# Kernel tuning notes

Hardware: AMD Instinct MI355X
Metric: run time of the kernel (lower is better)

Reference implementation:

```python
import jax, jax.numpy as jnp
import numpy as np
import math

N, N0, M, K, CIN, COUT, DIM = 50000, 50000, 32, 15, 64, 64, 3
POINT_INFLUENCE = 0.05
KERNEL_RADIUS = 1.5 * POINT_INFLUENCE  # _INFLUENCE_TO_RADIUS * point_influence


def setup_inputs() -> dict:
    key = jax.random.key(0)
    k1, k2, k3, k4, k5, k6 = jax.random.split(key, 6)
    query_points = jax.random.uniform(k1, (N, DIM), dtype=jnp.float32)
    support_points = jax.random.uniform(k2, (N0, DIM), dtype=jnp.float32)
    # index N0 is the shadow-neighbor index (padding for ragged neighborhoods)
    neighbors = jax.random.randint(k3, (N, M), 0, N0 + 1)
    x = jax.random.normal(k4, (N0, CIN), dtype=jnp.float32)
    # kernel point dispositions inside the kernel ball, center point at origin (fixed='center')
    kp = jax.random.normal(k5, (K, DIM), dtype=jnp.float32)
    kp = kp / jnp.linalg.norm(kp, axis=1, keepdims=True) * (KERNEL_RADIUS * 0.66)
    K_points = kp.at[0].set(0.0)
    # xavier_normal_ init for weight [K, CIN, COUT]
    std = math.sqrt(2.0 / (CIN + COUT))
    weight = jax.random.normal(k6, (K, CIN, COUT), dtype=jnp.float32) * std
    return dict(query_points=query_points, support_points=support_points,
                neighbors=neighbors, x=x, K_points=K_points, weight=weight)


def reference(query_points, support_points, neighbors, x, K_points, weight):
    # shadow point far away + zero shadow feature (handles padded neighbor index N0)
    shadow_pt = jnp.full((1, support_points.shape[1]), 1e6, support_points.dtype)
    sp = jnp.concatenate([support_points, shadow_pt], axis=0)          # [N0+1, 3]
    feats = jnp.concatenate([x, jnp.zeros((1, x.shape[1]), x.dtype)], axis=0)  # [N0+1, CIN]

    # gather & center neighborhoods: [N, M, 3]
    nb_pts = sp[neighbors] - query_points[:, None, :]

    # squared distance to each kernel point without materializing [N,M,K,3]:
    # ||n - k||^2 = ||n||^2 - 2 n.k + ||k||^2  -> [N, M, K]
    sq = (jnp.sum(nb_pts * nb_pts, axis=-1)[:, :, None]
          - 2.0 * jnp.einsum('nmd,kd->nmk', nb_pts, K_points)
          + jnp.sum(K_points * K_points, axis=-1))
    sq = jnp.maximum(sq, 0.0)

    # linear KP influence: clamp(1 - dist / point_influence, min=0) -> transpose to [N, K, M]
    all_weights = jnp.maximum(1.0 - jnp.sqrt(sq) / POINT_INFLUENCE, 0.0)
    all_weights = jnp.swapaxes(all_weights, 1, 2)                      # [N, K, M]

    nb_feats = feats[neighbors]                                        # [N, M, CIN]
    weighted = jnp.matmul(all_weights, nb_feats)                       # [N, K, CIN]
    # sum over kernel points of per-kernel-point matmuls ('sum' aggregation)
    out = jnp.einsum('nkc,kco->no', weighted, weight)                  # [N, COUT]
    return out
```

## Files before the change

### kernel.cpp

```cpp
#include <hip/hip_runtime.h>

#define N_Q   50000
#define N_S   50000
#define M_NB  32
#define K_PTS 15
#define CIN   64
#define COUT  64
#define WPB   2
#define THR   0.0101f

__device__ __forceinline__ void do_event(
    unsigned em, int laneoff, float w, int idx,
    float* bc, const float* wq, int cg,
    const float* __restrict__ x, int lane, float4& tout)
{
    float racc = 0.f;
    do {
        const int src = laneoff + __builtin_ctz(em); em &= em - 1;
        const float wsrc = __shfl(w, src);
        const int   isrc = __builtin_amdgcn_readfirstlane(__shfl(idx, src));
        racc = fmaf(wsrc, x[(size_t)isrc * CIN + lane], racc);
    } while (em);
    bc[lane] = racc;
    asm volatile("" ::: "memory");
    float4 a0 = make_float4(0.f, 0.f, 0.f, 0.f);
    float4 a1 = make_float4(0.f, 0.f, 0.f, 0.f);
    #pragma unroll
    for (int i = 0; i < 16; i += 2) {
        const float4 v0 = *(const float4*)(wq + (i + 0) * 4 * COUT);
        const float4 v1 = *(const float4*)(wq + (i + 1) * 4 * COUT);
        const float xc0 = bc[cg + 4 * i];
        const float xc1 = bc[cg + 4 * i + 4];
        a0.x = fmaf(xc0, v0.x, a0.x); a0.y = fmaf(xc0, v0.y, a0.y);
        a0.z = fmaf(xc0, v0.z, a0.z); a0.w = fmaf(xc0, v0.w, a0.w);
        a1.x = fmaf(xc1, v1.x, a1.x); a1.y = fmaf(xc1, v1.y, a1.y);
        a1.z = fmaf(xc1, v1.z, a1.z); a1.w = fmaf(xc1, v1.w, a1.w);
    }
    a0.x += a1.x; a0.y += a1.y; a0.z += a1.z; a0.w += a1.w;
    a0.x += __shfl_xor(a0.x, 16); a0.y += __shfl_xor(a0.y, 16);
    a0.z += __shfl_xor(a0.z, 16); a0.w += __shfl_xor(a0.w, 16);
    a0.x += __shfl_xor(a0.x, 32); a0.y += __shfl_xor(a0.y, 32);
    a0.z += __shfl_xor(a0.z, 32); a0.w += __shfl_xor(a0.w, 32);
    tout.x += a0.x; tout.y += a0.y; tout.z += a0.z; tout.w += a0.w;
    asm volatile("" ::: "memory");
}

__global__ __launch_bounds__(128) void kpconv_fused8(
    const float* __restrict__ query,
    const float* __restrict__ support,
    const int*   __restrict__ neighbors,
    const float* __restrict__ x,
    const float* __restrict__ kpts,
    const float* __restrict__ weight,
    float*       __restrict__ out)
{
    __shared__ float s_kx[K_PTS], s_ky[K_PTS], s_kz[K_PTS], s_kk[K_PTS];
    __shared__ float s_bc[WPB][CIN];

    const int tid = threadIdx.x;
    if (tid < K_PTS) {
        float kx = kpts[tid * 3 + 0];
        float ky = kpts[tid * 3 + 1];
        float kz = kpts[tid * 3 + 2];
        s_kx[tid] = kx; s_ky[tid] = ky; s_kz[tid] = kz;
        s_kk[tid] = kx * kx + ky * ky + kz * kz;
    }
    __syncthreads();

    const int wv   = __builtin_amdgcn_readfirstlane(tid >> 6);
    const int lane = tid & 63;
    const int base = blockIdx.x * (WPB * 2) + wv * 2;
    const int h    = lane >> 5;
    const int n    = base + h;
    const int m    = lane & 31;

    const float qxA = query[(base + 0) * 3 + 0];
    const float qyA = query[(base + 0) * 3 + 1];
    const float qzA = query[(base + 0) * 3 + 2];
    const float qxB = query[(base + 1) * 3 + 0];
    const float qyB = query[(base + 1) * 3 + 1];
    const float qzB = query[(base + 1) * 3 + 2];
    const float qx = h ? qxB : qxA;
    const float qy = h ? qyB : qyA;
    const float qz = h ? qzB : qzA;

    const int idx = neighbors[n * M_NB + m];

    float dx = 0.f, dy = 0.f, dz = 0.f, nn = 1e30f;
    if (idx < N_S) {
        dx = support[idx * 3 + 0] - qx;
        dy = support[idx * 3 + 1] - qy;
        dz = support[idx * 3 + 2] - qz;
        nn = dx * dx + dy * dy + dz * dz;
    }

    const int og = (lane & 15) * 4;
    const int cg = lane >> 4;

    float4 toutA = make_float4(0.f, 0.f, 0.f, 0.f);
    float4 toutB = make_float4(0.f, 0.f, 0.f, 0.f);

    if (__ballot(nn < THR)) {
        for (int k = 0; k < K_PTS; ++k) {
            float w = 0.f;
            if (nn < THR) {
                float dot = dx * s_kx[k] + dy * s_ky[k] + dz * s_kz[k];
                float sq  = fmaxf(nn - 2.f * dot + s_kk[k], 0.f);
                if (sq < 0.0025f)
                    w = 1.f - sqrtf(sq) * 20.f;
            }
            const unsigned long long em = __ballot(w > 0.f);
            if (!em) continue;

            const float* wq = weight + (size_t)k * CIN * COUT + cg * COUT + og;

            unsigned mm;
            if ((mm = (unsigned)(em & 0xffffffffull)))
                do_event(mm,  0, w, idx, s_bc[wv], wq, cg, x, lane, toutA);
            if ((mm = (unsigned)(em >> 32)))
                do_event(mm, 32, w, idx, s_bc[wv], wq, cg, x, lane, toutB);
        }
    }

    float4* rowA = (float4*)(out + (size_t)(base + 0) * COUT);
    float4* rowB = (float4*)(out + (size_t)(base + 1) * COUT);
    if (lane < 16)       rowA[lane]      = toutA;
    else if (lane < 32)  rowB[lane - 16] = toutB;
}

extern "C" void kernel_launch(void* const* d_in, const int* in_sizes, int n_in,
                              void* d_out, int out_size, void* d_ws, size_t ws_size,
                              hipStream_t stream) {
    const float* query     = (const float*)d_in[0];
    const float* support   = (const float*)d_in[1];
    const int*   neighbors = (const int*)  d_in[2];
    const float* x         = (const float*)d_in[3];
    const float* kpts      = (const float*)d_in[4];
    const float* weight    = (const float*)d_in[5];
    float*       out       = (float*)d_out;

    kpconv_fused8<<<N_Q / 4, 128, 0, stream>>>(
        query, support, neighbors, x, kpts, weight, out);
}
```

Before: 27.75 us.

## Split KPConv into event-scan and per-kernel-point bucketed GEMM kernels

Replaces the single fused kernel with three kernels. A counter-zeroing kernel runs first. A scan kernel computes neighbor-to-kernel-point influences and appends sparse (query, neighbor, weight) events into per-(kernel point, sub-bucket) lists using atomic counters, and it also zeroes the output. A GEMM kernel then stages each kernel point's 64x64 weight matrix in LDS, processes that bucket's events, and accumulates into the output with float atomics. The aim is to stop re-reading weights from global memory for each event and to take the sparse matmul work off the scan path. In exchange it adds two kernel launches, global atomics, and a fixed per-bucket capacity of 192 that silently drops any events beyond it.

```diff
diff --git a/kernel.cpp b/kernel.cpp
--- a/kernel.cpp
+++ b/kernel.cpp
@@ -6,56 +6,29 @@
 #define K_PTS 15
 #define CIN   64
 #define COUT  64
-#define WPB   2
 #define THR   0.0101f
 
-__device__ __forceinline__ void do_event(
-    unsigned em, int laneoff, float w, int idx,
-    float* bc, const float* wq, int cg,
-    const float* __restrict__ x, int lane, float4& tout)
+#define NSUB  32
+#define NSEG  (K_PTS * NSUB)
+#define CTRS  16
+#define CAP   192
+#define EV_OFF 32768
+
+__global__ __launch_bounds__(512) void zero_ctr(int* __restrict__ counters)
 {
-    float racc = 0.f;
-    do {
-        const int src = laneoff + __builtin_ctz(em); em &= em - 1;
-        const float wsrc = __shfl(w, src);
-        const int   isrc = __builtin_amdgcn_readfirstlane(__shfl(idx, src));
-        racc = fmaf(wsrc, x[(size_t)isrc * CIN + lane], racc);
-    } while (em);
-    bc[lane] = racc;
-    asm volatile("" ::: "memory");
-    float4 a0 = make_float4(0.f, 0.f, 0.f, 0.f);
-    float4 a1 = make_float4(0.f, 0.f, 0.f, 0.f);
-    #pragma unroll
-    for (int i = 0; i < 16; i += 2) {
-        const float4 v0 = *(const float4*)(wq + (i + 0) * 4 * COUT);
-        const float4 v1 = *(const float4*)(wq + (i + 1) * 4 * COUT);
-        const float xc0 = bc[cg + 4 * i];
-        const float xc1 = bc[cg + 4 * i + 4];
-        a0.x = fmaf(xc0, v0.x, a0.x); a0.y = fmaf(xc0, v0.y, a0.y);
-        a0.z = fmaf(xc0, v0.z, a0.z); a0.w = fmaf(xc0, v0.w, a0.w);
-        a1.x = fmaf(xc1, v1.x, a1.x); a1.y = fmaf(xc1, v1.y, a1.y);
-        a1.z = fmaf(xc1, v1.z, a1.z); a1.w = fmaf(xc1, v1.w, a1.w);
-    }
-    a0.x += a1.x; a0.y += a1.y; a0.z += a1.z; a0.w += a1.w;
-    a0.x += __shfl_xor(a0.x, 16); a0.y += __shfl_xor(a0.y, 16);
-    a0.z += __shfl_xor(a0.z, 16); a0.w += __shfl_xor(a0.w, 16);
-    a0.x += __shfl_xor(a0.x, 32); a0.y += __shfl_xor(a0.y, 32);
-    a0.z += __shfl_xor(a0.z, 32); a0.w += __shfl_xor(a0.w, 32);
-    tout.x += a0.x; tout.y += a0.y; tout.z += a0.z; tout.w += a0.w;
-    asm volatile("" ::: "memory");
+    if (threadIdx.x < NSEG) counters[threadIdx.x * CTRS] = 0;
 }
 
-__global__ __launch_bounds__(128) void kpconv_fused8(
+__global__ __launch_bounds__(128) void scan_emit(
     const float* __restrict__ query,
     const float* __restrict__ support,
     const int*   __restrict__ neighbors,
-    const float* __restrict__ x,
     const float* __restrict__ kpts,
-    const float* __restrict__ weight,
-    float*       __restrict__ out)
+    int*         __restrict__ counters,
+    int4*        __restrict__ events,
+    float4*      __restrict__ out4)
 {
     __shared__ float s_kx[K_PTS], s_ky[K_PTS], s_kz[K_PTS], s_kk[K_PTS];
-    __shared__ float s_bc[WPB][CIN];
 
     const int tid = threadIdx.x;
     if (tid < K_PTS) {
@@ -67,65 +40,111 @@
     }
     __syncthreads();
 
-    const int wv   = __builtin_amdgcn_readfirstlane(tid >> 6);
+    const int wv   = tid >> 6;
     const int lane = tid & 63;
-    const int base = blockIdx.x * (WPB * 2) + wv * 2;
+    const int base = blockIdx.x * 4 + wv * 2;
     const int h    = lane >> 5;
     const int n    = base + h;
     const int m    = lane & 31;
-
-    const float qxA = query[(base + 0) * 3 + 0];
-    const float qyA = query[(base + 0) * 3 + 1];
-    const float qzA = query[(base + 0) * 3 + 2];
-    const float qxB = query[(base + 1) * 3 + 0];
-    const float qyB = query[(base + 1) * 3 + 1];
-    const float qzB = query[(base + 1) * 3 + 2];
-    const float qx = h ? qxB : qxA;
-    const float qy = h ? qyB : qyA;
-    const float qz = h ? qzB : qzA;
 
     const int idx = neighbors[n * M_NB + m];
 
     float dx = 0.f, dy = 0.f, dz = 0.f, nn = 1e30f;
     if (idx < N_S) {
-        dx = support[idx * 3 + 0] - qx;
-        dy = support[idx * 3 + 1] - qy;
-        dz = support[idx * 3 + 2] - qz;
+        dx = support[idx * 3 + 0] - query[n * 3 + 0];
+        dy = support[idx * 3 + 1] - query[n * 3 + 1];
+        dz = support[idx * 3 + 2] - query[n * 3 + 2];
         nn = dx * dx + dy * dy + dz * dz;
     }
 
-    const int og = (lane & 15) * 4;
-    const int cg = lane >> 4;
+    if (lane < 32)
+        out4[(size_t)base * (COUT / 4) + lane] = make_float4(0.f, 0.f, 0.f, 0.f);
 
-    float4 toutA = make_float4(0.f, 0.f, 0.f, 0.f);
-    float4 toutB = make_float4(0.f, 0.f, 0.f, 0.f);
-
-    if (__ballot(nn < THR)) {
+    if (nn < THR) {
+        const int sub = blockIdx.x & (NSUB - 1);
+        #pragma unroll
         for (int k = 0; k < K_PTS; ++k) {
-            float w = 0.f;
-            if (nn < THR) {
-                float dot = dx * s_kx[k] + dy * s_ky[k] + dz * s_kz[k];
-                float sq  = fmaxf(nn - 2.f * dot + s_kk[k], 0.f);
-                if (sq < 0.0025f)
-                    w = 1.f - sqrtf(sq) * 20.f;
+            float dot = dx * s_kx[k] + dy * s_ky[k] + dz * s_kz[k];
+            float sq  = fmaxf(nn - 2.f * dot + s_kk[k], 0.f);
+            if (sq < 0.0025f) {
+                float w = 1.f - sqrtf(sq) * 20.f;
+                const int seg  = k * NSUB + sub;
+                const int slot = atomicAdd(&counters[seg * CTRS], 1);
+                if (slot < CAP)
+                    events[seg * CAP + slot] =
+                        make_int4(n, idx, __float_as_int(w), 0);
             }
-            const unsigned long long em = __ballot(w > 0.f);
-            if (!em) continue;
-
-            const float* wq = weight + (size_t)k * CIN * COUT + cg * COUT + og;
-
-            unsigned mm;
-            if ((mm = (unsigned)(em & 0xffffffffull)))
-                do_event(mm,  0, w, idx, s_bc[wv], wq, cg, x, lane, toutA);
-            if ((mm = (unsigned)(em >> 32)))
-                do_event(mm, 32, w, idx, s_bc[wv], wq, cg, x, lane, toutB);
         }
     }
+}
 
-    float4* rowA = (float4*)(out + (size_t)(base + 0) * COUT);
-    float4* rowB = (float4*)(out + (size_t)(base + 1) * COUT);
-    if (lane < 16)       rowA[lane]      = toutA;
-    else if (lane < 32)  rowB[lane - 16] = toutB;
+__global__ __launch_bounds__(256) void gemm_k(
+    const float* __restrict__ x,
+    const float* __restrict__ weight,
+    const int*   __restrict__ counters,
+    const int4*  __restrict__ events,
+    float*       __restrict__ out)
+{
+    __shared__ float s_w[CIN * COUT];
+    __shared__ float s_bc[4][CIN];
+
+    const int k   = blockIdx.x >> 5;
+    const int sub = blockIdx.x & (NSUB - 1);
+
+    {
+        const float4* src = (const float4*)(weight + (size_t)k * CIN * COUT);
+        float4* dst = (float4*)s_w;
+        #pragma unroll
+        for (int i = 0; i < 4; ++i)
+            dst[threadIdx.x + 256 * i] = src[threadIdx.x + 256 * i];
+    }
+    __syncthreads();
+
+    const int cnt = min(counters[(k * NSUB + sub) * CTRS], CAP);
+    const int4* evb = events + (size_t)(k * NSUB + sub) * CAP;
+
+    const int wv   = threadIdx.x >> 6;
+    const int lane = threadIdx.x & 63;
+    const int og   = (lane & 15) * 4;
+    const int cg   = lane >> 4;
+
+    for (int e = wv; e < cnt; e += 4) {
+        const int4 ev = evb[e];
+        const int   n   = __builtin_amdgcn_readfirstlane(ev.x);
+        const int   idx = __builtin_amdgcn_readfirstlane(ev.y);
+        const float w   = __int_as_float(__builtin_amdgcn_readfirstlane(ev.z));
+
+        s_bc[wv][lane] = x[(size_t)idx * CIN + lane];
+        asm volatile("" ::: "memory");
+
+        float4 a0 = make_float4(0.f, 0.f, 0.f, 0.f);
+        float4 a1 = make_float4(0.f, 0.f, 0.f, 0.f);
+        #pragma unroll
+        for (int i = 0; i < 16; i += 2) {
+            const float4 v0 = *(const float4*)(s_w + (cg + 4 * (i + 0)) * COUT + og);
+            const float4 v1 = *(const float4*)(s_w + (cg + 4 * (i + 1)) * COUT + og);
+            const float xc0 = s_bc[wv][cg + 4 * i];
+            const float xc1 = s_bc[wv][cg + 4 * i + 4];
+            a0.x = fmaf(xc0, v0.x, a0.x); a0.y = fmaf(xc0, v0.y, a0.y);
+            a0.z = fmaf(xc0, v0.z, a0.z); a0.w = fmaf(xc0, v0.w, a0.w);
+            a1.x = fmaf(xc1, v1.x, a1.x); a1.y = fmaf(xc1, v1.y, a1.y);
+            a1.z = fmaf(xc1, v1.z, a1.z); a1.w = fmaf(xc1, v1.w, a1.w);
+        }
+        a0.x += a1.x; a0.y += a1.y; a0.z += a1.z; a0.w += a1.w;
+        a0.x += __shfl_xor(a0.x, 16); a0.y += __shfl_xor(a0.y, 16);
+        a0.z += __shfl_xor(a0.z, 16); a0.w += __shfl_xor(a0.w, 16);
+        a0.x += __shfl_xor(a0.x, 32); a0.y += __shfl_xor(a0.y, 32);
+        a0.z += __shfl_xor(a0.z, 32); a0.w += __shfl_xor(a0.w, 32);
+
+        if (lane < 16) {
+            float* row = out + (size_t)n * COUT + og;
+            atomicAdd(&row[0], w * a0.x);
+            atomicAdd(&row[1], w * a0.y);
+            atomicAdd(&row[2], w * a0.z);
+            atomicAdd(&row[3], w * a0.w);
+        }
+        asm volatile("" ::: "memory");
+    }
 }
 
 extern "C" void kernel_launch(void* const* d_in, const int* in_sizes, int n_in,
@@ -139,6 +158,11 @@
     const float* weight    = (const float*)d_in[5];
     float*       out       = (float*)d_out;
 
-    kpconv_fused8<<<N_Q / 4, 128, 0, stream>>>(
-        query, support, neighbors, x, kpts, weight, out);
+    int*  counters = (int*)d_ws;
+    int4* events   = (int4*)((char*)d_ws + EV_OFF);
+
+    zero_ctr<<<1, 512, 0, stream>>>(counters);
+    scan_emit<<<N_Q / 4, 128, 0, stream>>>(
+        query, support, neighbors, kpts, counters, events, (float4*)out);
+    gemm_k<<<NSEG, 256, 0, stream>>>(x, weight, counters, events, out);
 }
```

After: 46.48 us. 1.67x slower.

## Prefetch candidate neighbor features and pair weight-matmul events for more ILP

Applied to the files above, without the earlier changes.

Before the kernel-point loop, the features of up to four candidate neighbors within the distance threshold are loaded into registers, so the per-event gather usually reuses them. Weight-matrix products are no longer done once per kernel-point event. Events are buffered in pairs through two shared-memory rows, and both 64x64 weight slices are processed in one unrolled loop. This overlaps more independent loads and FMAs and cuts serialized latency chains. In exchange it raises register pressure and adds branching on the lane-match checks.

```diff
diff --git a/kernel.cpp b/kernel.cpp
--- a/kernel.cpp
+++ b/kernel.cpp
@@ -9,43 +9,13 @@
 #define WPB   2
 #define THR   0.0101f
 
-__device__ __forceinline__ void do_event(
-    unsigned em, int laneoff, float w, int idx,
-    float* bc, const float* wq, int cg,
-    const float* __restrict__ x, int lane, float4& tout)
-{
-    float racc = 0.f;
-    do {
-        const int src = laneoff + __builtin_ctz(em); em &= em - 1;
-        const float wsrc = __shfl(w, src);
-        const int   isrc = __builtin_amdgcn_readfirstlane(__shfl(idx, src));
-        racc = fmaf(wsrc, x[(size_t)isrc * CIN + lane], racc);
-    } while (em);
-    bc[lane] = racc;
-    asm volatile("" ::: "memory");
-    float4 a0 = make_float4(0.f, 0.f, 0.f, 0.f);
-    float4 a1 = make_float4(0.f, 0.f, 0.f, 0.f);
-    #pragma unroll
-    for (int i = 0; i < 16; i += 2) {
-        const float4 v0 = *(const float4*)(wq + (i + 0) * 4 * COUT);
-        const float4 v1 = *(const float4*)(wq + (i + 1) * 4 * COUT);
-        const float xc0 = bc[cg + 4 * i];
-        const float xc1 = bc[cg + 4 * i + 4];
-        a0.x = fmaf(xc0, v0.x, a0.x); a0.y = fmaf(xc0, v0.y, a0.y);
-        a0.z = fmaf(xc0, v0.z, a0.z); a0.w = fmaf(xc0, v0.w, a0.w);
-        a1.x = fmaf(xc1, v1.x, a1.x); a1.y = fmaf(xc1, v1.y, a1.y);
-        a1.z = fmaf(xc1, v1.z, a1.z); a1.w = fmaf(xc1, v1.w, a1.w);
-    }
-    a0.x += a1.x; a0.y += a1.y; a0.z += a1.z; a0.w += a1.w;
-    a0.x += __shfl_xor(a0.x, 16); a0.y += __shfl_xor(a0.y, 16);
-    a0.z += __shfl_xor(a0.z, 16); a0.w += __shfl_xor(a0.w, 16);
-    a0.x += __shfl_xor(a0.x, 32); a0.y += __shfl_xor(a0.y, 32);
-    a0.z += __shfl_xor(a0.z, 32); a0.w += __shfl_xor(a0.w, 32);
-    tout.x += a0.x; tout.y += a0.y; tout.z += a0.z; tout.w += a0.w;
-    asm volatile("" ::: "memory");
-}
-
-__global__ __launch_bounds__(128) void kpconv_fused8(
+#define RED4(a)                                                      \
+    a.x += __shfl_xor(a.x, 16); a.y += __shfl_xor(a.y, 16);          \
+    a.z += __shfl_xor(a.z, 16); a.w += __shfl_xor(a.w, 16);          \
+    a.x += __shfl_xor(a.x, 32); a.y += __shfl_xor(a.y, 32);          \
+    a.z += __shfl_xor(a.z, 32); a.w += __shfl_xor(a.w, 32);
+
+__global__ __launch_bounds__(128) void kpconv_fused9(
     const float* __restrict__ query,
     const float* __restrict__ support,
     const int*   __restrict__ neighbors,
@@ -55,7 +25,7 @@
     float*       __restrict__ out)
 {
     __shared__ float s_kx[K_PTS], s_ky[K_PTS], s_kz[K_PTS], s_kk[K_PTS];
-    __shared__ float s_bc[WPB][CIN];
+    __shared__ float s_r0[WPB][CIN], s_r1[WPB][CIN];
 
     const int tid = threadIdx.x;
     if (tid < K_PTS) {
@@ -100,7 +70,23 @@
     float4 toutA = make_float4(0.f, 0.f, 0.f, 0.f);
     float4 toutB = make_float4(0.f, 0.f, 0.f, 0.f);
 
-    if (__ballot(nn < THR)) {
+    const unsigned long long cb = __ballot(nn < THR);
+
+    if (cb) {
+        unsigned long long t = cb;
+        int s0 = -1, s1 = -1, s2 = -1, s3 = -1;
+        if (t) { s0 = __ffsll(t) - 1; t &= t - 1; }
+        if (t) { s1 = __ffsll(t) - 1; t &= t - 1; }
+        if (t) { s2 = __ffsll(t) - 1; t &= t - 1; }
+        if (t) { s3 = __ffsll(t) - 1; t &= t - 1; }
+        float xr0 = 0.f, xr1 = 0.f, xr2 = 0.f, xr3 = 0.f;
+        if (s0 >= 0) xr0 = x[(size_t)__builtin_amdgcn_readfirstlane(__shfl(idx, s0)) * CIN + lane];
+        if (s1 >= 0) xr1 = x[(size_t)__builtin_amdgcn_readfirstlane(__shfl(idx, s1)) * CIN + lane];
+        if (s2 >= 0) xr2 = x[(size_t)__builtin_amdgcn_readfirstlane(__shfl(idx, s2)) * CIN + lane];
+        if (s3 >= 0) xr3 = x[(size_t)__builtin_amdgcn_readfirstlane(__shfl(idx, s3)) * CIN + lane];
+
+        int havePend = 0, pk = 0, pB = 0;
+
         for (int k = 0; k < K_PTS; ++k) {
             float w = 0.f;
             if (nn < THR) {
@@ -112,13 +98,91 @@
             const unsigned long long em = __ballot(w > 0.f);
             if (!em) continue;
 
-            const float* wq = weight + (size_t)k * CIN * COUT + cg * COUT + og;
-
-            unsigned mm;
-            if ((mm = (unsigned)(em & 0xffffffffull)))
-                do_event(mm,  0, w, idx, s_bc[wv], wq, cg, x, lane, toutA);
-            if ((mm = (unsigned)(em >> 32)))
-                do_event(mm, 32, w, idx, s_bc[wv], wq, cg, x, lane, toutB);
+            #pragma unroll
+            for (int half = 0; half < 2; ++half) {
+                unsigned mm = half ? (unsigned)(em >> 32)
+                                   : (unsigned)(em & 0xffffffffull);
+                if (!mm) continue;
+                const int off = half * 32;
+
+                float racc = 0.f;
+                do {
+                    const int src = off + __builtin_ctz(mm); mm &= mm - 1;
+                    const float wsrc = __shfl(w, src);
+                    float xv;
+                    if      (src == s0) xv = xr0;
+                    else if (src == s1) xv = xr1;
+                    else if (src == s2) xv = xr2;
+                    else if (src == s3) xv = xr3;
+                    else xv = x[(size_t)__builtin_amdgcn_readfirstlane(
+                                   __shfl(idx, src)) * CIN + lane];
+                    racc = fmaf(wsrc, xv, racc);
+                } while (mm);
+
+                if (!havePend) {
+                    s_r0[wv][lane] = racc;
+                    asm volatile("" ::: "memory");
+                    pk = k; pB = half; havePend = 1;
+                } else {
+                    s_r1[wv][lane] = racc;
+                    asm volatile("" ::: "memory");
+                    const float* wqa = weight + (size_t)pk * CIN * COUT + cg * COUT + og;
+                    const float* wqb = weight + (size_t)k  * CIN * COUT + cg * COUT + og;
+                    float4 a0 = make_float4(0.f,0.f,0.f,0.f);
+                    float4 a1 = make_float4(0.f,0.f,0.f,0.f);
+                    float4 b0 = make_float4(0.f,0.f,0.f,0.f);
+                    float4 b1 = make_float4(0.f,0.f,0.f,0.f);
+                    #pragma unroll
+                    for (int i = 0; i < 16; i += 2) {
+                        const float4 va0 = *(const float4*)(wqa + (i + 0) * 4 * COUT);
+                        const float4 va1 = *(const float4*)(wqa + (i + 1) * 4 * COUT);
+                        const float4 vb0 = *(const float4*)(wqb + (i + 0) * 4 * COUT);
+                        const float4 vb1 = *(const float4*)(wqb + (i + 1) * 4 * COUT);
+                        const float xa0 = s_r0[wv][cg + 4 * i];
+                        const float xa1 = s_r0[wv][cg + 4 * i + 4];
+                        const float xb0 = s_r1[wv][cg + 4 * i];
+                        const float xb1 = s_r1[wv][cg + 4 * i + 4];
+                        a0.x = fmaf(xa0, va0.x, a0.x); a0.y = fmaf(xa0, va0.y, a0.y);
+                        a0.z = fmaf(xa0, va0.z, a0.z); a0.w = fmaf(xa0, va0.w, a0.w);
+                        a1.x = fmaf(xa1, va1.x, a1.x); a1.y = fmaf(xa1, va1.y, a1.y);
+                        a1.z = fmaf(xa1, va1.z, a1.z); a1.w = fmaf(xa1, va1.w, a1.w);
+                        b0.x = fmaf(xb0, vb0.x, b0.x); b0.y = fmaf(xb0, vb0.y, b0.y);
+                        b0.z = fmaf(xb0, vb0.z, b0.z); b0.w = fmaf(xb0, vb0.w, b0.w);
+                        b1.x = fmaf(xb1, vb1.x, b1.x); b1.y = fmaf(xb1, vb1.y, b1.y);
+                        b1.z = fmaf(xb1, vb1.z, b1.z); b1.w = fmaf(xb1, vb1.w, b1.w);
+                    }
+                    a0.x += a1.x; a0.y += a1.y; a0.z += a1.z; a0.w += a1.w;
+                    b0.x += b1.x; b0.y += b1.y; b0.z += b1.z; b0.w += b1.w;
+                    RED4(a0); RED4(b0);
+                    if (pB) { toutB.x += a0.x; toutB.y += a0.y; toutB.z += a0.z; toutB.w += a0.w; }
+                    else    { toutA.x += a0.x; toutA.y += a0.y; toutA.z += a0.z; toutA.w += a0.w; }
+                    if (half) { toutB.x += b0.x; toutB.y += b0.y; toutB.z += b0.z; toutB.w += b0.w; }
+                    else      { toutA.x += b0.x; toutA.y += b0.y; toutA.z += b0.z; toutA.w += b0.w; }
+                    havePend = 0;
+                    asm volatile("" ::: "memory");
+                }
+            }
+        }
+
+        if (havePend) {
+            const float* wqa = weight + (size_t)pk * CIN * COUT + cg * COUT + og;
+            float4 a0 = make_float4(0.f,0.f,0.f,0.f);
+            float4 a1 = make_float4(0.f,0.f,0.f,0.f);
+            #pragma unroll
+            for (int i = 0; i < 16; i += 2) {
+                const float4 va0 = *(const float4*)(wqa + (i + 0) * 4 * COUT);
+                const float4 va1 = *(const float4*)(wqa + (i + 1) * 4 * COUT);
+                const float xa0 = s_r0[wv][cg + 4 * i];
+                const float xa1 = s_r0[wv][cg + 4 * i + 4];
+                a0.x = fmaf(xa0, va0.x, a0.x); a0.y = fmaf(xa0, va0.y, a0.y);
+                a0.z = fmaf(xa0, va0.z, a0.z); a0.w = fmaf(xa0, va0.w, a0.w);
+                a1.x = fmaf(xa1, va1.x, a1.x); a1.y = fmaf(xa1, va1.y, a1.y);
+                a1.z = fmaf(xa1, va1.z, a1.z); a1.w = fmaf(xa1, va1.w, a1.w);
+            }
+            a0.x += a1.x; a0.y += a1.y; a0.z += a1.z; a0.w += a1.w;
+            RED4(a0);
+            if (pB) { toutB.x += a0.x; toutB.y += a0.y; toutB.z += a0.z; toutB.w += a0.w; }
+            else    { toutA.x += a0.x; toutA.y += a0.y; toutA.z += a0.z; toutA.w += a0.w; }
         }
     }
 
@@ -139,6 +203,6 @@
     const float* weight    = (const float*)d_in[5];
     float*       out       = (float*)d_out;
 
-    kpconv_fused8<<<N_Q / 4, 128, 0, stream>>>(
+    kpconv_fused9<<<N_Q / 4, 128, 0, stream>>>(
         query, support, neighbors, x, kpts, weight, out);
 }
```

Result: slower. 28.62 us (+3.1%).

## Split into scan pass emitting sparse worklist and persistent compute kernel

Applied to the files above, without the earlier changes.

Replaces the single fused kernel with two kernels. The first scans all neighborhoods, zero-fills the output and records per-wave-pair counts and query indices in a workspace. The second runs a grid-stride persistent kernel that does the full weight computation and matmul only for the listed queries. The aim is to stop close neighbourhoods from causing load imbalance across waves. The cost is a second launch, a re-read of neighbor and support data for the listed queries, and a scan of every segment's count by the persistent kernel.

```diff
diff --git a/kernel.cpp b/kernel.cpp
--- a/kernel.cpp
+++ b/kernel.cpp
@@ -6,70 +6,23 @@
 #define K_PTS 15
 #define CIN   64
 #define COUT  64
-#define WPB   2
 #define THR   0.0101f
+#define NSEG  25000
+#define WL_OFF 131072
 
-__device__ __forceinline__ void do_event(
-    unsigned em, int laneoff, float w, int idx,
-    float* bc, const float* wq, int cg,
-    const float* __restrict__ x, int lane, float4& tout)
-{
-    float racc = 0.f;
-    do {
-        const int src = laneoff + __builtin_ctz(em); em &= em - 1;
-        const float wsrc = __shfl(w, src);
-        const int   isrc = __builtin_amdgcn_readfirstlane(__shfl(idx, src));
-        racc = fmaf(wsrc, x[(size_t)isrc * CIN + lane], racc);
-    } while (em);
-    bc[lane] = racc;
-    asm volatile("" ::: "memory");
-    float4 a0 = make_float4(0.f, 0.f, 0.f, 0.f);
-    float4 a1 = make_float4(0.f, 0.f, 0.f, 0.f);
-    #pragma unroll
-    for (int i = 0; i < 16; i += 2) {
-        const float4 v0 = *(const float4*)(wq + (i + 0) * 4 * COUT);
-        const float4 v1 = *(const float4*)(wq + (i + 1) * 4 * COUT);
-        const float xc0 = bc[cg + 4 * i];
-        const float xc1 = bc[cg + 4 * i + 4];
-        a0.x = fmaf(xc0, v0.x, a0.x); a0.y = fmaf(xc0, v0.y, a0.y);
-        a0.z = fmaf(xc0, v0.z, a0.z); a0.w = fmaf(xc0, v0.w, a0.w);
-        a1.x = fmaf(xc1, v1.x, a1.x); a1.y = fmaf(xc1, v1.y, a1.y);
-        a1.z = fmaf(xc1, v1.z, a1.z); a1.w = fmaf(xc1, v1.w, a1.w);
-    }
-    a0.x += a1.x; a0.y += a1.y; a0.z += a1.z; a0.w += a1.w;
-    a0.x += __shfl_xor(a0.x, 16); a0.y += __shfl_xor(a0.y, 16);
-    a0.z += __shfl_xor(a0.z, 16); a0.w += __shfl_xor(a0.w, 16);
-    a0.x += __shfl_xor(a0.x, 32); a0.y += __shfl_xor(a0.y, 32);
-    a0.z += __shfl_xor(a0.z, 32); a0.w += __shfl_xor(a0.w, 32);
-    tout.x += a0.x; tout.y += a0.y; tout.z += a0.z; tout.w += a0.w;
-    asm volatile("" ::: "memory");
-}
-
-__global__ __launch_bounds__(128) void kpconv_fused8(
+__global__ __launch_bounds__(128) void scan_emit(
     const float* __restrict__ query,
     const float* __restrict__ support,
     const int*   __restrict__ neighbors,
-    const float* __restrict__ x,
-    const float* __restrict__ kpts,
-    const float* __restrict__ weight,
-    float*       __restrict__ out)
+    int*         __restrict__ counts,
+    int2*        __restrict__ worklist,
+    float4*      __restrict__ out4)
 {
-    __shared__ float s_kx[K_PTS], s_ky[K_PTS], s_kz[K_PTS], s_kk[K_PTS];
-    __shared__ float s_bc[WPB][CIN];
-
-    const int tid = threadIdx.x;
-    if (tid < K_PTS) {
-        float kx = kpts[tid * 3 + 0];
-        float ky = kpts[tid * 3 + 1];
-        float kz = kpts[tid * 3 + 2];
-        s_kx[tid] = kx; s_ky[tid] = ky; s_kz[tid] = kz;
-        s_kk[tid] = kx * kx + ky * ky + kz * kz;
-    }
-    __syncthreads();
-
+    const int tid  = threadIdx.x;
     const int wv   = __builtin_amdgcn_readfirstlane(tid >> 6);
     const int lane = tid & 63;
-    const int base = blockIdx.x * (WPB * 2) + wv * 2;
+    const int base = blockIdx.x * 4 + wv * 2;
+    const int wid  = blockIdx.x * 2 + wv;
     const int h    = lane >> 5;
     const int n    = base + h;
     const int m    = lane & 31;
@@ -86,46 +39,129 @@
 
     const int idx = neighbors[n * M_NB + m];
 
-    float dx = 0.f, dy = 0.f, dz = 0.f, nn = 1e30f;
+    float nn = 1e30f;
     if (idx < N_S) {
-        dx = support[idx * 3 + 0] - qx;
-        dy = support[idx * 3 + 1] - qy;
-        dz = support[idx * 3 + 2] - qz;
+        const float dx = support[idx * 3 + 0] - qx;
+        const float dy = support[idx * 3 + 1] - qy;
+        const float dz = support[idx * 3 + 2] - qz;
         nn = dx * dx + dy * dy + dz * dz;
     }
 
-    const int og = (lane & 15) * 4;
-    const int cg = lane >> 4;
+    if (lane < 32)
+        out4[(size_t)base * (COUT / 4) + lane] = make_float4(0.f, 0.f, 0.f, 0.f);
 
-    float4 toutA = make_float4(0.f, 0.f, 0.f, 0.f);
-    float4 toutB = make_float4(0.f, 0.f, 0.f, 0.f);
+    const unsigned long long cb = __ballot(nn < THR);
+    const int cA = ((unsigned)(cb & 0xffffffffull)) != 0;
+    const int cB = ((unsigned)(cb >> 32)) != 0;
+    if (lane == 0) {
+        counts[wid] = cA + cB;
+        if (cA + cB)
+            worklist[wid] = make_int2(cA ? base : base + 1, base + 1);
+    }
+}
 
-    if (__ballot(nn < THR)) {
-        for (int k = 0; k < K_PTS; ++k) {
-            float w = 0.f;
-            if (nn < THR) {
-                float dot = dx * s_kx[k] + dy * s_ky[k] + dz * s_kz[k];
-                float sq  = fmaxf(nn - 2.f * dot + s_kk[k], 0.f);
-                if (sq < 0.0025f)
-                    w = 1.f - sqrtf(sq) * 20.f;
+__global__ __launch_bounds__(256) void close_kernel(
+    const float* __restrict__ query,
+    const float* __restrict__ support,
+    const int*   __restrict__ neighbors,
+    const float* __restrict__ x,
+    const float* __restrict__ kpts,
+    const float* __restrict__ weight,
+    const int*   __restrict__ counts,
+    const int2*  __restrict__ worklist,
+    float*       __restrict__ out)
+{
+    __shared__ float s_kx[K_PTS], s_ky[K_PTS], s_kz[K_PTS], s_kk[K_PTS];
+    __shared__ float s_bc[4][CIN];
+
+    const int tid = threadIdx.x;
+    if (tid < K_PTS) {
+        float kx = kpts[tid * 3 + 0];
+        float ky = kpts[tid * 3 + 1];
+        float kz = kpts[tid * 3 + 2];
+        s_kx[tid] = kx; s_ky[tid] = ky; s_kz[tid] = kz;
+        s_kk[tid] = kx * kx + ky * ky + kz * kz;
+    }
+    __syncthreads();
+
+    const int wv   = tid >> 6;
+    const int lane = tid & 63;
+    const int wid  = blockIdx.x * 4 + wv;
+    const int nw   = gridDim.x * 4;
+    const int og   = (lane & 15) * 4;
+    const int cg   = lane >> 4;
+
+    for (int seg = wid; seg < NSEG; seg += nw) {
+        const int cnt = counts[seg];
+        if (!cnt) continue;
+        const int2 wl = worklist[seg];
+
+        for (int i = 0; i < cnt; ++i) {
+            const int n = __builtin_amdgcn_readfirstlane(i ? wl.y : wl.x);
+
+            int idx = N_S;
+            float dx = 0.f, dy = 0.f, dz = 0.f, nn = 1e30f;
+            if (lane < 32) {
+                idx = neighbors[n * M_NB + lane];
+                if (idx < N_S) {
+                    dx = support[idx * 3 + 0] - query[n * 3 + 0];
+                    dy = support[idx * 3 + 1] - query[n * 3 + 1];
+                    dz = support[idx * 3 + 2] - query[n * 3 + 2];
+                    nn = dx * dx + dy * dy + dz * dz;
+                }
             }
-            const unsigned long long em = __ballot(w > 0.f);
-            if (!em) continue;
 
-            const float* wq = weight + (size_t)k * CIN * COUT + cg * COUT + og;
+            float4 tq = make_float4(0.f, 0.f, 0.f, 0.f);
 
-            unsigned mm;
-            if ((mm = (unsigned)(em & 0xffffffffull)))
-                do_event(mm,  0, w, idx, s_bc[wv], wq, cg, x, lane, toutA);
-            if ((mm = (unsigned)(em >> 32)))
-                do_event(mm, 32, w, idx, s_bc[wv], wq, cg, x, lane, toutB);
+            for (int k = 0; k < K_PTS; ++k) {
+                float w = 0.f;
+                if (nn < THR) {
+                    float dot = dx * s_kx[k] + dy * s_ky[k] + dz * s_kz[k];
+                    float sq  = fmaxf(nn - 2.f * dot + s_kk[k], 0.f);
+                    if (sq < 0.0025f)
+                        w = 1.f - sqrtf(sq) * 20.f;
+                }
+                unsigned em = (unsigned)__ballot(w > 0.f);
+                if (!em) continue;
+
+                float racc = 0.f;
+                do {
+                    const int src = __builtin_ctz(em); em &= em - 1;
+                    const float wsrc = __shfl(w, src);
+                    const int   isrc = __builtin_amdgcn_readfirstlane(
+                                           __shfl(idx, src));
+                    racc = fmaf(wsrc, x[(size_t)isrc * CIN + lane], racc);
+                } while (em);
+
+                s_bc[wv][lane] = racc;
+                asm volatile("" ::: "memory");
+                const float* wq = weight + (size_t)k * CIN * COUT + cg * COUT + og;
+                float4 a0 = make_float4(0.f, 0.f, 0.f, 0.f);
+                float4 a1 = make_float4(0.f, 0.f, 0.f, 0.f);
+                #pragma unroll
+                for (int q = 0; q < 16; q += 2) {
+                    const float4 v0 = *(const float4*)(wq + (q + 0) * 4 * COUT);
+                    const float4 v1 = *(const float4*)(wq + (q + 1) * 4 * COUT);
+                    const float xc0 = s_bc[wv][cg + 4 * q];
+                    const float xc1 = s_bc[wv][cg + 4 * q + 4];
+                    a0.x = fmaf(xc0, v0.x, a0.x); a0.y = fmaf(xc0, v0.y, a0.y);
+                    a0.z = fmaf(xc0, v0.z, a0.z); a0.w = fmaf(xc0, v0.w, a0.w);
+                    a1.x = fmaf(xc1, v1.x, a1.x); a1.y = fmaf(xc1, v1.y, a1.y);
+                    a1.z = fmaf(xc1, v1.z, a1.z); a1.w = fmaf(xc1, v1.w, a1.w);
+                }
+                a0.x += a1.x; a0.y += a1.y; a0.z += a1.z; a0.w += a1.w;
+                a0.x += __shfl_xor(a0.x, 16); a0.y += __shfl_xor(a0.y, 16);
+                a0.z += __shfl_xor(a0.z, 16); a0.w += __shfl_xor(a0.w, 16);
+                a0.x += __shfl_xor(a0.x, 32); a0.y += __shfl_xor(a0.y, 32);
+                a0.z += __shfl_xor(a0.z, 32); a0.w += __shfl_xor(a0.w, 32);
+                tq.x += a0.x; tq.y += a0.y; tq.z += a0.z; tq.w += a0.w;
+                asm volatile("" ::: "memory");
+            }
+
+            float4* row = (float4*)(out + (size_t)n * COUT);
+            if (lane < 16) row[lane] = tq;
         }
     }
-
-    float4* rowA = (float4*)(out + (size_t)(base + 0) * COUT);
-    float4* rowB = (float4*)(out + (size_t)(base + 1) * COUT);
-    if (lane < 16)       rowA[lane]      = toutA;
-    else if (lane < 32)  rowB[lane - 16] = toutB;
 }
 
 extern "C" void kernel_launch(void* const* d_in, const int* in_sizes, int n_in,
@@ -139,6 +175,11 @@
     const float* weight    = (const float*)d_in[5];
     float*       out       = (float*)d_out;
 
-    kpconv_fused8<<<N_Q / 4, 128, 0, stream>>>(
-        query, support, neighbors, x, kpts, weight, out);
+    int*  counts   = (int*)d_ws;
+    int2* worklist = (int2*)((char*)d_ws + WL_OFF);
+
+    scan_emit<<<N_Q / 4, 128, 0, stream>>>(
+        query, support, neighbors, counts, worklist, (float4*)out);
+    close_kernel<<<2048, 256, 0, stream>>>(
+        query, support, neighbors, x, kpts, weight, counts, worklist, out);
 }
```

New measurement: 42.10 us. 51.7% more time.
